# Kernel tuning notes

Hardware: AMD Instinct MI355X
Metric: run time of the kernel (lower is better)

The kernel has to match this reference:

```python
import jax, jax.numpy as jnp
import numpy as np

N, NQ, NV, NE = 4, 256, 512, 256


def setup_inputs() -> dict:
    key = jax.random.key(0)
    ks = jax.random.split(key, 6)
    scale = 1.0 / np.sqrt(NE)
    return {
        "query": jax.random.normal(ks[0], (N, NQ, NE), dtype=jnp.float32),
        "context": jax.random.normal(ks[1], (N, NV, NE), dtype=jnp.float32),
        "memory": jax.random.normal(ks[2], (N, NV, NE), dtype=jnp.float32),
        "w_logit": jax.random.normal(ks[3], (NE,), dtype=jnp.float32) * scale,
        "b_logit": jnp.zeros((), dtype=jnp.float32),
        "temp": jnp.ones((), dtype=jnp.float32),
        "w_reduce": jax.random.normal(ks[4], (NE, NE), dtype=jnp.float32) * scale,
        "b_reduce": jnp.zeros((NE,), dtype=jnp.float32),
    }


def reference(query, context, memory, w_logit, b_logit, temp, w_reduce, b_reduce):
    # Additive (Bahdanau) attention, single-head branch of the torch module.
    # qc: [N, nQ, nV, nE] -- the large broadcast-add + tanh intermediate
    qc = jnp.tanh(query[:, :, None, :] + context[:, None, :, :])
    # fc_logit: Linear(nE -> 1), squeeze last dim -> [N, nQ, nV]
    logits = jnp.einsum("nqve,e->nqv", qc, w_logit) + b_logit
    probs = jax.nn.softmax(logits / temp, axis=2)
    # bmm(probs, memory) -> [N, nQ, nE], then leaky_relu (torch default slope 0.01)
    heads = jax.nn.leaky_relu(jnp.einsum("nqv,nve->nqe", probs, memory), negative_slope=0.01)
    # fc_reduceheads: Linear(nE -> nE), torch semantics y = x @ W.T + b
    return heads @ w_reduce.T + b_reduce
```

## Files before the change

kernel.cpp:

```cpp
#include <hip/hip_runtime.h>
#include <math.h>

#define N_B   4
#define NQ_   256
#define NV_   512
#define NE_   256
#define QT_   2
#define NW_   8
#define BLK_  512

#define QSCALE 2.8853900817779268f

__device__ __forceinline__ float wave_reduce_sum(float v) {
#pragma unroll
    for (int m = 32; m > 0; m >>= 1) v += __shfl_xor(v, m, 64);
    return v;
}

__global__ __launch_bounds__(256) void transpose_C(const float* __restrict__ C,
                                                   float* __restrict__ CT) {
    __shared__ float tile[64][65];
    const int n = blockIdx.z, v0 = blockIdx.x * 64, e0 = blockIdx.y * 64;
    const int col = threadIdx.x & 63, row4 = threadIdx.x >> 6;
    const float* src = C + ((size_t)n * NV_ + v0) * NE_ + e0;
#pragma unroll
    for (int r = 0; r < 16; ++r) {
        const int vl = row4 + r * 4;
        tile[vl][col] = src[(size_t)vl * NE_ + col] * QSCALE;
    }
    __syncthreads();
    float* dst = CT + ((size_t)n * NE_ + e0) * NV_ + v0;
#pragma unroll
    for (int r = 0; r < 16; ++r) {
        const int el = row4 + r * 4;
        dst[(size_t)el * NV_ + col] = tile[col][el];
    }
}

__global__ __launch_bounds__(256) void transpose_W(const float* __restrict__ W,
                                                   float* __restrict__ WT) {
    __shared__ float tile[64][65];
    const int r0 = blockIdx.x * 64, c0 = blockIdx.y * 64;
    const int col = threadIdx.x & 63, row4 = threadIdx.x >> 6;
    const float* src = W + (size_t)r0 * NE_ + c0;
#pragma unroll
    for (int r = 0; r < 16; ++r) {
        const int rl = row4 + r * 4;
        tile[rl][col] = src[(size_t)rl * NE_ + col];
    }
    __syncthreads();
    float* dst = WT + (size_t)c0 * NE_ + r0;
#pragma unroll
    for (int r = 0; r < 16; ++r) {
        const int cl = row4 + r * 4;
        dst[(size_t)cl * NE_ + col] = tile[col][cl];
    }
}

__global__ __launch_bounds__(BLK_) void attn_main(
    const float* __restrict__ Q,
    const float* __restrict__ CT,
    const float* __restrict__ M,
    const float* __restrict__ WL,
    const float* __restrict__ TEMP,
    const float* __restrict__ WRT,
    const float* __restrict__ BR,
    float* __restrict__ OUT)
{
    const int n   = blockIdx.y;
    const int q0  = blockIdx.x * QT_;
    const int tid = threadIdx.x;
    const int wv  = tid >> 6;
    const int ln  = tid & 63;

    __shared__ __align__(16) float4 s_qw[NE_];
    __shared__ __align__(16) float  s_prob[QT_][NV_];
    __shared__ __align__(16) float  s_part[NW_][QT_][NE_];
    __shared__ __align__(16) float  s_heads[QT_][NE_];

    if (tid < NE_) {
        const float a = Q[((size_t)n * NQ_ + q0) * NE_ + tid] * QSCALE;
        const float b = Q[((size_t)n * NQ_ + q0 + 1) * NE_ + tid] * QSCALE;
        s_qw[tid] = make_float4(a, b, WL[tid], 0.0f);
    }
    __syncthreads();

    {
        const float* ct = CT + (size_t)n * NE_ * NV_ + wv * 64 + ln;
        float acc0 = 0.0f, acc1 = 0.0f;
#pragma unroll 8
        for (int e = 0; e < NE_; ++e) {
            const float c = ct[(size_t)e * NV_];
            const float4 qw = s_qw[e];
            const float p0 = __builtin_amdgcn_exp2f(c + qw.x);
            const float p1 = __builtin_amdgcn_exp2f(c + qw.y);
            const float r0 = __builtin_amdgcn_rcpf(1.0f + p0);
            const float r1 = __builtin_amdgcn_rcpf(1.0f + p1);
            acc0 = fmaf(qw.z, r0, acc0);
            acc1 = fmaf(qw.z, r1, acc1);
        }
        s_prob[0][wv * 64 + ln] = acc0;
        s_prob[1][wv * 64 + ln] = acc1;
    }
    __syncthreads();

    if (wv < QT_) {
        const int q = wv;
        const float scale = -2.0f / TEMP[0];
        float l[NV_ / 64];
        float mx = -1e30f;
#pragma unroll
        for (int k = 0; k < NV_ / 64; ++k) {
            l[k] = s_prob[q][ln + 64 * k] * scale;
            mx = fmaxf(mx, l[k]);
        }
#pragma unroll
        for (int m = 32; m > 0; m >>= 1) mx = fmaxf(mx, __shfl_xor(mx, m, 64));
        float sum = 0.0f;
#pragma unroll
        for (int k = 0; k < NV_ / 64; ++k) {
            l[k] = __expf(l[k] - mx);
            sum += l[k];
        }
        sum = wave_reduce_sum(sum);
        const float inv = 1.0f / sum;
#pragma unroll
        for (int k = 0; k < NV_ / 64; ++k) s_prob[q][ln + 64 * k] = l[k] * inv;
    }
    __syncthreads();

    {
        const float4* M4 = (const float4*)(M + (size_t)n * NV_ * NE_);
        float4 h0 = make_float4(0.f, 0.f, 0.f, 0.f);
        float4 h1 = make_float4(0.f, 0.f, 0.f, 0.f);
        const int v0 = wv * (NV_ / NW_);
#pragma unroll 4
        for (int v = v0; v < v0 + NV_ / NW_; ++v) {
            const float4 m = M4[v * (NE_ / 4) + ln];
            const float p0 = s_prob[0][v];
            const float p1 = s_prob[1][v];
            h0.x = fmaf(p0, m.x, h0.x); h0.y = fmaf(p0, m.y, h0.y);
            h0.z = fmaf(p0, m.z, h0.z); h0.w = fmaf(p0, m.w, h0.w);
            h1.x = fmaf(p1, m.x, h1.x); h1.y = fmaf(p1, m.y, h1.y);
            h1.z = fmaf(p1, m.z, h1.z); h1.w = fmaf(p1, m.w, h1.w);
        }
        ((float4*)s_part[wv][0])[ln] = h0;
        ((float4*)s_part[wv][1])[ln] = h1;
    }
    __syncthreads();

    {
        const int t = tid >> 8, e = tid & (NE_ - 1);
        float s = 0.0f;
#pragma unroll
        for (int w = 0; w < NW_; ++w) s += s_part[w][t][e];
        s_heads[t][e] = (s > 0.0f) ? s : 0.01f * s;
    }
    __syncthreads();

    {
        const int t  = wv >> 2;
        const int ep = ((wv & 3) << 6) + ln;
        const float* wrt = WRT + ep;
        float acc = 0.0f;
#pragma unroll 8
        for (int e = 0; e < NE_; ++e)
            acc = fmaf(s_heads[t][e], wrt[(size_t)e * NE_], acc);
        OUT[((size_t)n * NQ_ + q0 + t) * NE_ + ep] = acc + BR[ep];
    }
}

extern "C" void kernel_launch(void* const* d_in, const int* in_sizes, int n_in,
                              void* d_out, int out_size, void* d_ws, size_t ws_size,
                              hipStream_t stream) {
    const float* Q  = (const float*)d_in[0];
    const float* C  = (const float*)d_in[1];
    const float* M  = (const float*)d_in[2];
    const float* WL = (const float*)d_in[3];
    const float* T  = (const float*)d_in[5];
    const float* WR = (const float*)d_in[6];
    const float* BR = (const float*)d_in[7];
    float* OUT = (float*)d_out;

    float* CT  = (float*)d_ws;
    float* WRT = CT + (size_t)N_B * NE_ * NV_;

    dim3 gtc(NV_ / 64, NE_ / 64, N_B);
    transpose_C<<<gtc, 256, 0, stream>>>(C, CT);
    dim3 gtw(NE_ / 64, NE_ / 64);
    transpose_W<<<gtw, 256, 0, stream>>>(WR, WRT);

    dim3 grid(NQ_ / QT_, N_B);
    attn_main<<<grid, BLK_, 0, stream>>>(Q, CT, M, WL, T, WRT, BR, OUT);
}
```

Before: 119.2 us.

## Split fused attention kernel into separate logits and softmax-output kernels

The single fused kernel is split in two. The first computes the tanh-based logits over a 3D grid, with each block handling 4 queries and 64 values and the embedding dimension divided across waves. The second reads those logits from global memory, then runs softmax, the memory bmm and the output projection using 256-thread blocks. The aim is more parallelism and reuse of each context load across more queries in the expensive transcendental phase, at the cost of an extra launch and a round trip of the logits through global memory.

```diff
diff --git a/kernel.cpp b/kernel.cpp
--- a/kernel.cpp
+++ b/kernel.cpp
@@ -5,9 +5,6 @@
 #define NQ_   256
 #define NV_   512
 #define NE_   256
-#define QT_   2
-#define NW_   8
-#define BLK_  512
 
 #define QSCALE 2.8853900817779268f
 
@@ -57,61 +54,85 @@
     }
 }
 
-__global__ __launch_bounds__(BLK_) void attn_main(
+#define QTA 4
+__global__ __launch_bounds__(256, 8) void logits_kernel(
     const float* __restrict__ Q,
     const float* __restrict__ CT,
+    const float* __restrict__ WL,
+    float* __restrict__ S)
+{
+    const int n  = blockIdx.z;
+    const int q0 = blockIdx.y * QTA;
+    const int v0 = blockIdx.x * 64;
+    const int tid = threadIdx.x;
+    const int wv = tid >> 6, ln = tid & 63;
+
+    __shared__ __align__(16) float s_q[NE_][QTA];
+    __shared__ float s_w[NE_];
+    __shared__ float s_part[4][QTA][64];
+
+    {
+        const int e = tid;
+        s_w[e] = WL[e];
+#pragma unroll
+        for (int j = 0; j < QTA; ++j)
+            s_q[e][j] = Q[((size_t)n * NQ_ + q0 + j) * NE_ + e] * QSCALE;
+    }
+    __syncthreads();
+
+    const float* ct = CT + (size_t)n * NE_ * NV_ + v0 + ln;
+    float acc0 = 0.f, acc1 = 0.f, acc2 = 0.f, acc3 = 0.f;
+    const int e0 = wv * 64;
+#pragma unroll 4
+    for (int e = e0; e < e0 + 64; ++e) {
+        const float c = ct[(size_t)e * NV_];
+        const float4 q4 = *(const float4*)s_q[e];
+        const float w = s_w[e];
+        acc0 = fmaf(w, __builtin_amdgcn_rcpf(1.0f + __builtin_amdgcn_exp2f(c + q4.x)), acc0);
+        acc1 = fmaf(w, __builtin_amdgcn_rcpf(1.0f + __builtin_amdgcn_exp2f(c + q4.y)), acc1);
+        acc2 = fmaf(w, __builtin_amdgcn_rcpf(1.0f + __builtin_amdgcn_exp2f(c + q4.z)), acc2);
+        acc3 = fmaf(w, __builtin_amdgcn_rcpf(1.0f + __builtin_amdgcn_exp2f(c + q4.w)), acc3);
+    }
+    s_part[wv][0][ln] = acc0;
+    s_part[wv][1][ln] = acc1;
+    s_part[wv][2][ln] = acc2;
+    s_part[wv][3][ln] = acc3;
+    __syncthreads();
+
+    {
+        const int j = tid >> 6, l = tid & 63;
+        const float s = s_part[0][j][l] + s_part[1][j][l]
+                      + s_part[2][j][l] + s_part[3][j][l];
+        S[((size_t)n * NQ_ + q0 + j) * NV_ + v0 + l] = s;
+    }
+}
+
+#define QTB 2
+__global__ __launch_bounds__(256) void attn_out(
+    const float* __restrict__ S,
     const float* __restrict__ M,
-    const float* __restrict__ WL,
     const float* __restrict__ TEMP,
     const float* __restrict__ WRT,
     const float* __restrict__ BR,
     float* __restrict__ OUT)
 {
-    const int n   = blockIdx.y;
-    const int q0  = blockIdx.x * QT_;
+    const int n  = blockIdx.y;
+    const int q0 = blockIdx.x * QTB;
     const int tid = threadIdx.x;
-    const int wv  = tid >> 6;
-    const int ln  = tid & 63;
-
-    __shared__ __align__(16) float4 s_qw[NE_];
-    __shared__ __align__(16) float  s_prob[QT_][NV_];
-    __shared__ __align__(16) float  s_part[NW_][QT_][NE_];
-    __shared__ __align__(16) float  s_heads[QT_][NE_];
-
-    if (tid < NE_) {
-        const float a = Q[((size_t)n * NQ_ + q0) * NE_ + tid] * QSCALE;
-        const float b = Q[((size_t)n * NQ_ + q0 + 1) * NE_ + tid] * QSCALE;
-        s_qw[tid] = make_float4(a, b, WL[tid], 0.0f);
-    }
-    __syncthreads();
-
-    {
-        const float* ct = CT + (size_t)n * NE_ * NV_ + wv * 64 + ln;
-        float acc0 = 0.0f, acc1 = 0.0f;
-#pragma unroll 8
-        for (int e = 0; e < NE_; ++e) {
-            const float c = ct[(size_t)e * NV_];
-            const float4 qw = s_qw[e];
-            const float p0 = __builtin_amdgcn_exp2f(c + qw.x);
-            const float p1 = __builtin_amdgcn_exp2f(c + qw.y);
-            const float r0 = __builtin_amdgcn_rcpf(1.0f + p0);
-            const float r1 = __builtin_amdgcn_rcpf(1.0f + p1);
-            acc0 = fmaf(qw.z, r0, acc0);
-            acc1 = fmaf(qw.z, r1, acc1);
-        }
-        s_prob[0][wv * 64 + ln] = acc0;
-        s_prob[1][wv * 64 + ln] = acc1;
-    }
-    __syncthreads();
-
-    if (wv < QT_) {
-        const int q = wv;
+    const int wv = tid >> 6, ln = tid & 63;
+
+    __shared__ __align__(16) float s_prob[QTB][NV_];
+    __shared__ __align__(16) float s_part[4][QTB][NE_];
+    __shared__ __align__(16) float s_heads[QTB][NE_];
+
+    if (wv < QTB) {
         const float scale = -2.0f / TEMP[0];
+        const float* srow = S + ((size_t)n * NQ_ + q0 + wv) * NV_;
         float l[NV_ / 64];
         float mx = -1e30f;
 #pragma unroll
         for (int k = 0; k < NV_ / 64; ++k) {
-            l[k] = s_prob[q][ln + 64 * k] * scale;
+            l[k] = srow[ln + 64 * k] * scale;
             mx = fmaxf(mx, l[k]);
         }
 #pragma unroll
@@ -125,7 +146,7 @@
         sum = wave_reduce_sum(sum);
         const float inv = 1.0f / sum;
 #pragma unroll
-        for (int k = 0; k < NV_ / 64; ++k) s_prob[q][ln + 64 * k] = l[k] * inv;
+        for (int k = 0; k < NV_ / 64; ++k) s_prob[wv][ln + 64 * k] = l[k] * inv;
     }
     __syncthreads();
 
@@ -133,9 +154,9 @@
         const float4* M4 = (const float4*)(M + (size_t)n * NV_ * NE_);
         float4 h0 = make_float4(0.f, 0.f, 0.f, 0.f);
         float4 h1 = make_float4(0.f, 0.f, 0.f, 0.f);
-        const int v0 = wv * (NV_ / NW_);
+        const int v0 = wv * (NV_ / 4);
 #pragma unroll 4
-        for (int v = v0; v < v0 + NV_ / NW_; ++v) {
+        for (int v = v0; v < v0 + NV_ / 4; ++v) {
             const float4 m = M4[v * (NE_ / 4) + ln];
             const float p0 = s_prob[0][v];
             const float p1 = s_prob[1][v];
@@ -149,24 +170,27 @@
     }
     __syncthreads();
 
-    {
-        const int t = tid >> 8, e = tid & (NE_ - 1);
-        float s = 0.0f;
-#pragma unroll
-        for (int w = 0; w < NW_; ++w) s += s_part[w][t][e];
+#pragma unroll
+    for (int i = tid; i < QTB * NE_; i += 256) {
+        const int t = i >> 8, e = i & (NE_ - 1);
+        const float s = s_part[0][t][e] + s_part[1][t][e]
+                      + s_part[2][t][e] + s_part[3][t][e];
         s_heads[t][e] = (s > 0.0f) ? s : 0.01f * s;
     }
     __syncthreads();
 
     {
-        const int t  = wv >> 2;
-        const int ep = ((wv & 3) << 6) + ln;
-        const float* wrt = WRT + ep;
-        float acc = 0.0f;
+        const float* w = WRT + tid;
+        float a0 = 0.f, a1 = 0.f;
 #pragma unroll 8
-        for (int e = 0; e < NE_; ++e)
-            acc = fmaf(s_heads[t][e], wrt[(size_t)e * NE_], acc);
-        OUT[((size_t)n * NQ_ + q0 + t) * NE_ + ep] = acc + BR[ep];
+        for (int e = 0; e < NE_; ++e) {
+            const float wv_ = w[(size_t)e * NE_];
+            a0 = fmaf(s_heads[0][e], wv_, a0);
+            a1 = fmaf(s_heads[1][e], wv_, a1);
+        }
+        const float b = BR[tid];
+        OUT[((size_t)n * NQ_ + q0) * NE_ + tid]     = a0 + b;
+        OUT[((size_t)n * NQ_ + q0 + 1) * NE_ + tid] = a1 + b;
     }
 }
 
@@ -184,12 +208,16 @@
 
     float* CT  = (float*)d_ws;
     float* WRT = CT + (size_t)N_B * NE_ * NV_;
+    float* S   = WRT + (size_t)NE_ * NE_;
 
     dim3 gtc(NV_ / 64, NE_ / 64, N_B);
     transpose_C<<<gtc, 256, 0, stream>>>(C, CT);
     dim3 gtw(NE_ / 64, NE_ / 64);
     transpose_W<<<gtw, 256, 0, stream>>>(WR, WRT);
 
-    dim3 grid(NQ_ / QT_, N_B);
-    attn_main<<<grid, BLK_, 0, stream>>>(Q, CT, M, WL, T, WRT, BR, OUT);
-}
+    dim3 ga(NV_ / 64, NQ_ / QTA, N_B);
+    logits_kernel<<<ga, 256, 0, stream>>>(Q, CT, WL, S);
+
+    dim3 gb(NQ_ / QTB, N_B);
+    attn_out<<<gb, 256, 0, stream>>>(S, M, T, WRT, BR, OUT);
+}
```

Measured after the change: 122.5 us. 1.03x slower.
